# Kernel tuning notes

Measured on AMD Instinct MI355X. Metric: run time of the kernel, lower is better.

Reference implementation:

```python
import jax, jax.numpy as jnp
import numpy as np

B, T, D = 4, 2048, 768
H, HD = 8, 96          # n_heads, head_dim
NB = HD // 24          # number of 24-dim Leech blocks per head
NEG_INF = -1e30


def _leech_kernel_24():
    # QR of the bidiagonal/circulant base matrix, as in generate_leech_kernel
    base = np.zeros((24, 24), dtype=np.float32)
    for i in range(23):
        base[i, i] = 2.0
        base[i, i + 1] = 2.0
    base[23, 23] = 2.0
    base[23, 0] = -2.0
    q, _ = np.linalg.qr(base)
    return jnp.asarray(q, dtype=jnp.float32)


def setup_inputs() -> dict:
    key = jax.random.key(0)
    k1, k2, k3 = jax.random.split(key, 3)
    x = jax.random.normal(k1, (B, T, D), dtype=jnp.float32)
    w_qkv = jax.random.normal(k2, (3 * D, D), dtype=jnp.float32) * (D ** -0.5)
    w_out = jax.random.normal(k3, (D, D), dtype=jnp.float32) * (D ** -0.5)
    kernel = _leech_kernel_24()
    return {"x": x, "w_qkv": w_qkv, "w_out": w_out, "kernel": kernel}


def reference(x, w_qkv, w_out, kernel):
    Bx, Tx, Dx = x.shape
    scale = HD ** -0.5
    # qkv projection (bias=False)
    qkv = jnp.einsum('btd,ed->bte', x, w_qkv)            # [B,T,3D]
    qkv = qkv.reshape(Bx, Tx, 3, H, HD).transpose(2, 0, 3, 1, 4)  # [3,B,H,T,HD]
    q, k, v = qkv[0], qkv[1], qkv[2]
    # per-24-block orthogonal Leech rotation on q and k
    q = jnp.einsum('bhtni,ij->bhtnj', q.reshape(Bx, H, Tx, NB, 24), kernel)
    k = jnp.einsum('bhtni,ij->bhtnj', k.reshape(Bx, H, Tx, NB, 24), kernel)
    q = q.reshape(Bx, H, Tx, HD)
    k = k.reshape(Bx, H, Tx, HD)
    # causal attention (manual softmax; dropout inactive in eval)
    scores = jnp.einsum('bhqd,bhkd->bhqk', q, k) * scale
    causal = jnp.tril(jnp.ones((Tx, Tx), dtype=bool))
    scores = jnp.where(causal[None, None], scores, NEG_INF)
    attn = jax.nn.softmax(scores, axis=-1)
    out = jnp.einsum('bhqk,bhkd->bhqd', attn, v)          # [B,H,T,HD]
    out = out.transpose(0, 2, 1, 3).reshape(Bx, Tx, Dx)
    return jnp.einsum('btd,ed->bte', out, w_out)
```

## Files before the change

### kernel.cpp

```cpp
#include <hip/hip_runtime.h>
#include <cstdint>
#include <cstddef>

#define Bq 4
#define T 2048
#define Dm 768
#define H 8
#define HD 96
#define BH 32
#define QEL ((size_t)BH*T*HD)
#define KEL ((size_t)BH*T*128)
#define PSTRIDE 98304
#define QS 0.14724703336f
#define KVB 64
#define M0 12.0f

typedef unsigned int u32;
typedef unsigned long long u64;
typedef _Float16 f16x8 __attribute__((ext_vector_type(8)));
typedef _Float16 f16x4 __attribute__((ext_vector_type(4)));
typedef float f32x4 __attribute__((ext_vector_type(4)));

__global__ __launch_bounds__(256)
void cvt_tile(const float* __restrict__ in, _Float16* __restrict__ out)
{
    const int tid  = threadIdx.x;
    const int lane = tid & 63;
    const int gw   = (blockIdx.x * 256 + tid) >> 6;
    const int kc   = gw % 96;
    const int row  = (gw / 96) * 64 + lane;
    const float4 a = *reinterpret_cast<const float4*>(in + (size_t)row * 768 + kc * 8);
    const float4 b = *reinterpret_cast<const float4*>(in + (size_t)row * 768 + kc * 8 + 4);
    f16x8 h;
    h[0] = (_Float16)a.x; h[1] = (_Float16)a.y; h[2] = (_Float16)a.z; h[3] = (_Float16)a.w;
    h[4] = (_Float16)b.x; h[5] = (_Float16)b.y; h[6] = (_Float16)b.z; h[7] = (_Float16)b.w;
    *reinterpret_cast<f16x8*>(
        out + (size_t)(row >> 7) * PSTRIDE + (size_t)kc * 1024 + (row & 127) * 8) = h;
}

template <bool SCATTER>
__global__ __launch_bounds__(256)
void gemm_mfma(const _Float16* __restrict__ At, const _Float16* __restrict__ Bt,
               _Float16* __restrict__ qb, _Float16* __restrict__ kpd,
               _Float16* __restrict__ vtb, float* __restrict__ C,
               int N, int nx)
{
    constexpr int NSTEP = Dm / 64;
    __shared__ _Float16 As[2][8 * 128 * 8];
    __shared__ _Float16 Bs[2][8 * 128 * 8];

    const int tid  = threadIdx.x;
    const int lane = tid & 63;
    const int wid  = tid >> 6;
    const int li   = lane & 15;
    const int lg   = lane >> 4;
    const int wr   = wid >> 1;
    const int wc   = wid & 1;

    const int qch = gridDim.x >> 3;
    const int id  = (blockIdx.x & 7) * qch + (blockIdx.x >> 3);
    const int m0  = (id / nx) * 128;
    const int n0  = (id % nx) * 128;

    const _Float16* baseA = At + (size_t)(m0 >> 7) * PSTRIDE;
    const _Float16* baseB = Bt + (size_t)(n0 >> 7) * PSTRIDE;

    f32x4 acc[4][4];
#pragma unroll
    for (int i = 0; i < 4; ++i)
#pragma unroll
        for (int j = 0; j < 4; ++j) acc[i][j] = (f32x4)0.f;

    auto STAGE = [&](int t, int b) {
        const _Float16* pa = baseA + (t << 13);
        const _Float16* pb = baseB + (t << 13);
#pragma unroll
        for (int i = 0; i < 4; ++i) {
            const int s = wid * 64 + i * 256;
            __builtin_amdgcn_global_load_lds(
                (const __attribute__((address_space(1))) void*)(pa + (size_t)(s + lane) * 8),
                (__attribute__((address_space(3))) void*)&As[b][s * 8], 16, 0, 0);
            __builtin_amdgcn_global_load_lds(
                (const __attribute__((address_space(1))) void*)(pb + (size_t)(s + lane) * 8),
                (__attribute__((address_space(3))) void*)&Bs[b][s * 8], 16, 0, 0);
        }
    };

    STAGE(0, 0);
    for (int t = 0; t < NSTEP; ++t) {
        const int p = t & 1;
        if (t + 1 < NSTEP) {
            STAGE(t + 1, p ^ 1);
            asm volatile("s_waitcnt vmcnt(8)" ::: "memory");
        } else {
            asm volatile("s_waitcnt vmcnt(0)" ::: "memory");
        }
        __builtin_amdgcn_s_barrier();

#pragma unroll
        for (int c = 0; c < 2; ++c) {
            f16x8 af[4], bf[4];
#pragma unroll
            for (int i = 0; i < 4; ++i)
                af[i] = *reinterpret_cast<const f16x8*>(
                    &As[p][((c * 4 + lg) * 128 + wr * 64 + i * 16 + li) * 8]);
#pragma unroll
            for (int j = 0; j < 4; ++j)
                bf[j] = *reinterpret_cast<const f16x8*>(
                    &Bs[p][((c * 4 + lg) * 128 + wc * 64 + j * 16 + li) * 8]);
            __builtin_amdgcn_s_setprio(1);
#pragma unroll
            for (int i = 0; i < 4; ++i)
#pragma unroll
                for (int j = 0; j < 4; ++j)
                    acc[i][j] = __builtin_amdgcn_mfma_f32_16x16x32_f16(
                        af[i], bf[j], acc[i][j], 0, 0, 0);
            __builtin_amdgcn_s_setprio(0);
        }

        asm volatile("s_waitcnt lgkmcnt(0)" ::: "memory");
        __builtin_amdgcn_s_barrier();
    }

#pragma unroll
    for (int i = 0; i < 4; ++i) {
#pragma unroll
        for (int r = 0; r < 4; ++r) {
            const int m = m0 + wr * 64 + i * 16 + lg * 4 + r;
            if (SCATTER) {
                const int b_ = m >> 11, t_ = m & 2047;
#pragma unroll
                for (int j = 0; j < 4; ++j) {
                    const int e = n0 + wc * 64 + j * 16 + li;
                    const int c = e / Dm;
                    const int rem = e - c * Dm;
                    const int h = rem / HD;
                    const int d = rem - h * HD;
                    const size_t bhx = (size_t)(b_ * H + h);
                    const float v = acc[i][j][r];
                    if (c == 0)
                        qb[(bhx * T + t_) * HD + d] = (_Float16)(v * QS);
                    else if (c == 1)
                        kpd[(bhx * T + t_) * 128 + d] = (_Float16)v;
                    else
                        vtb[(bhx * 96 + d) * T + t_] = (_Float16)v;
                }
            } else {
#pragma unroll
                for (int j = 0; j < 4; ++j) {
                    const int n = n0 + wc * 64 + j * 16 + li;
                    C[(size_t)m * N + n] = acc[i][j][r];
                }
            }
        }
    }
}

__global__ __launch_bounds__(256)
void attn_mfma(const _Float16* __restrict__ QG, const _Float16* __restrict__ KG,
               const _Float16* __restrict__ VtG, _Float16* __restrict__ aoh)
{
    __shared__ __align__(16) _Float16 Klds[2][64 * 128];
    __shared__ __align__(16) _Float16 Vlds[2][112 * 64];
    __shared__ __align__(16) _Float16 Pl[4][16][72];

    const int tid  = threadIdx.x;
    const int lane = tid & 63;
    const int wid  = tid >> 6;
    const int lg   = lane >> 4;
    const int li   = lane & 15;

    const int bh = blockIdx.x & 31;
    const int i  = blockIdx.x >> 5;
    const int qt0 = i, qt1 = 31 - i;

    {
        const u32 one2 = 0x3C003C00u;
        u32* vp0 = reinterpret_cast<u32*>(&Vlds[0][96 * 64]);
        u32* vp1 = reinterpret_cast<u32*>(&Vlds[1][96 * 64]);
#pragma unroll
        for (int k = tid; k < 512; k += 256) {
            const u32 v = (k < 32) ? one2 : 0u;
            vp0[k] = v; vp1[k] = v;
        }
    }
    __syncthreads();

    f16x8 qf0[3], qf1[3];
    {
        const _Float16* qr0 = QG + ((size_t)bh * T + qt0 * 64 + wid * 16 + li) * HD;
        const _Float16* qr1 = QG + ((size_t)bh * T + qt1 * 64 + wid * 16 + li) * HD;
#pragma unroll
        for (int ch = 0; ch < 3; ++ch) {
            qf0[ch] = *reinterpret_cast<const f16x8*>(qr0 + ch * 32 + lg * 8);
            qf1[ch] = *reinterpret_cast<const f16x8*>(qr1 + ch * 32 + lg * 8);
        }
    }

    const int swz = (li & 7) << 3;
    int kofs[4][3], vofs[7][2];
#pragma unroll
    for (int kt = 0; kt < 4; ++kt)
#pragma unroll
        for (int ch = 0; ch < 3; ++ch)
            kofs[kt][ch] = (kt * 16 + li) * 128 + ((ch * 32 + lg * 8) ^ swz);
#pragma unroll
    for (int dt = 0; dt < 7; ++dt)
#pragma unroll
        for (int pc = 0; pc < 2; ++pc)
            vofs[dt][pc] = (dt * 16 + li) * 64 + ((pc * 32 + lg * 8) ^ swz);

    const int rK = lane >> 4;
    const int cK = (lane & 15) * 8;
    const int rV = lane >> 3;
    const int cV = (lane & 7) * 8;
    auto STAGE = [&](int kb, int b) {
#pragma unroll
        for (int ii = 0; ii < 4; ++ii) {
            const int r  = wid * 16 + ii * 4 + rK;
            const int c0 = cK ^ (((ii * 4 + rK) & 7) << 3);
            const _Float16* src = KG + ((size_t)(bh * T + kb + r)) * 128 + c0;
            __builtin_amdgcn_global_load_lds(
                (const __attribute__((address_space(1))) void*)src,
                (__attribute__((address_space(3))) void*)&Klds[b][(wid * 16 + ii * 4) * 128],
                16, 0, 0);
        }
#pragma unroll
        for (int jj = 0; jj < 3; ++jj) {
            const int r  = wid * 24 + jj * 8 + rV;
            const int c0 = cV ^ (rV << 3);
            const _Float16* src = VtG + ((size_t)(bh * 96 + r)) * T + kb + c0;
            __builtin_amdgcn_global_load_lds(
                (const __attribute__((address_space(1))) void*)src,
                (__attribute__((address_space(3))) void*)&Vlds[b][(wid * 24 + jj * 8) * 64],
                16, 0, 0);
        }
    };

    f32x4 acc0[7], acc1[7];
#pragma unroll
    for (int dt = 0; dt < 7; ++dt) { acc0[dt] = (f32x4)0.f; acc1[dt] = (f32x4)0.f; }

    auto ROUND_FULL = [&](const f16x8 (&qf)[3], f32x4 (&acc)[7],
                          int p, int nextkb) {
        STAGE(nextkb, p ^ 1);
        asm volatile("s_waitcnt vmcnt(7)" ::: "memory");
        __builtin_amdgcn_s_barrier();

        const _Float16* Kb = &Klds[p][0];
        const _Float16* Vb = &Vlds[p][0];

        f16x8 kf[4][3];
#pragma unroll
        for (int kt = 0; kt < 4; ++kt)
#pragma unroll
            for (int ch = 0; ch < 3; ++ch)
                kf[kt][ch] = *reinterpret_cast<const f16x8*>(Kb + kofs[kt][ch]);

        f32x4 st[4];
        __builtin_amdgcn_s_setprio(1);
#pragma unroll
        for (int kt = 0; kt < 4; ++kt) {
            st[kt] = (f32x4)(-M0);
#pragma unroll
            for (int ch = 0; ch < 3; ++ch)
                st[kt] = __builtin_amdgcn_mfma_f32_16x16x32_f16(
                    kf[kt][ch], qf[ch], st[kt], 0, 0, 0);
        }
        __builtin_amdgcn_s_setprio(0);

#pragma unroll
        for (int kt = 0; kt < 4; ++kt) {
            const auto a = __builtin_amdgcn_cvt_pkrtz(
                __builtin_amdgcn_exp2f(st[kt][0]),
                __builtin_amdgcn_exp2f(st[kt][1]));
            const auto b = __builtin_amdgcn_cvt_pkrtz(
                __builtin_amdgcn_exp2f(st[kt][2]),
                __builtin_amdgcn_exp2f(st[kt][3]));
            const u64 w = (u64)__builtin_bit_cast(u32, a) |
                          ((u64)__builtin_bit_cast(u32, b) << 32);
            *reinterpret_cast<u64*>(&Pl[wid][li][kt * 16 + lg * 4]) = w;
        }

#pragma unroll
        for (int pc = 0; pc < 2; ++pc) {
            const f16x8 pf = *reinterpret_cast<const f16x8*>(
                &Pl[wid][li][pc * 32 + lg * 8]);
            __builtin_amdgcn_s_setprio(1);
#pragma unroll
            for (int dt = 0; dt < 7; ++dt) {
                const f16x8 vf = *reinterpret_cast<const f16x8*>(Vb + vofs[dt][pc]);
                acc[dt] = __builtin_amdgcn_mfma_f32_16x16x32_f16(
                    pf, vf, acc[dt], 0, 0, 0);
            }
            __builtin_amdgcn_s_setprio(0);
        }

        asm volatile("s_waitcnt lgkmcnt(0)" ::: "memory");
        __builtin_amdgcn_s_barrier();
    };

    auto ROUND_DIAG = [&](int kb, int q0w, const f16x8 (&qf)[3], f32x4 (&acc)[7],
                          int p, int nextkb, bool has_next) {
        if (has_next) {
            STAGE(nextkb, p ^ 1);
            asm volatile("s_waitcnt vmcnt(7)" ::: "memory");
        } else {
            asm volatile("s_waitcnt vmcnt(0)" ::: "memory");
        }
        __builtin_amdgcn_s_barrier();

        const _Float16* Kb = &Klds[p][0];
        const _Float16* Vb = &Vlds[p][0];
        const int nkt = min(4, ((q0w + 15 - kb) >> 4) + 1);

        f16x8 kf[4][3];
#pragma unroll
        for (int kt = 0; kt < 4; ++kt)
            if (kt < nkt) {
#pragma unroll
                for (int ch = 0; ch < 3; ++ch)
                    kf[kt][ch] = *reinterpret_cast<const f16x8*>(Kb + kofs[kt][ch]);
            }

        f32x4 st[4];
        __builtin_amdgcn_s_setprio(1);
#pragma unroll
        for (int kt = 0; kt < 4; ++kt) {
            st[kt] = (f32x4)(-M0);
            if (kt < nkt) {
#pragma unroll
                for (int ch = 0; ch < 3; ++ch)
                    st[kt] = __builtin_amdgcn_mfma_f32_16x16x32_f16(
                        kf[kt][ch], qf[ch], st[kt], 0, 0, 0);
            }
        }
        __builtin_amdgcn_s_setprio(0);

        const int qg = q0w + li;
#pragma unroll
        for (int kt = 0; kt < 4; ++kt)
            if (kt < nkt && kb + kt * 16 + 15 > q0w) {
#pragma unroll
                for (int rr = 0; rr < 4; ++rr) {
                    const int kg = kb + kt * 16 + lg * 4 + rr;
                    if (kg > qg) st[kt][rr] = -1e30f;
                }
            }

#pragma unroll
        for (int kt = 0; kt < 4; ++kt)
            if (kt < nkt) {
                const auto a = __builtin_amdgcn_cvt_pkrtz(
                    __builtin_amdgcn_exp2f(st[kt][0]),
                    __builtin_amdgcn_exp2f(st[kt][1]));
                const auto b = __builtin_amdgcn_cvt_pkrtz(
                    __builtin_amdgcn_exp2f(st[kt][2]),
                    __builtin_amdgcn_exp2f(st[kt][3]));
                const u64 w = (u64)__builtin_bit_cast(u32, a) |
                              ((u64)__builtin_bit_cast(u32, b) << 32);
                *reinterpret_cast<u64*>(&Pl[wid][li][kt * 16 + lg * 4]) = w;
            }
        if (nkt & 1)
            *reinterpret_cast<u64*>(&Pl[wid][li][nkt * 16 + lg * 4]) = 0ull;

        const int npc = (nkt + 1) >> 1;
#pragma unroll
        for (int pc = 0; pc < 2; ++pc)
            if (pc < npc) {
                const f16x8 pf = *reinterpret_cast<const f16x8*>(
                    &Pl[wid][li][pc * 32 + lg * 8]);
                __builtin_amdgcn_s_setprio(1);
#pragma unroll
                for (int dt = 0; dt < 7; ++dt) {
                    const f16x8 vf = *reinterpret_cast<const f16x8*>(Vb + vofs[dt][pc]);
                    acc[dt] = __builtin_amdgcn_mfma_f32_16x16x32_f16(
                        pf, vf, acc[dt], 0, 0, 0);
                }
                __builtin_amdgcn_s_setprio(0);
            }

        asm volatile("s_waitcnt lgkmcnt(0)" ::: "memory");
        __builtin_amdgcn_s_barrier();
    };

    STAGE(0, 0);
    const int q0w0 = qt0 * 64 + wid * 16;
    const int q0w1 = qt1 * 64 + wid * 16;
    int r = 0;
    for (int t = 0; t < i; ++t, ++r)
        ROUND_FULL(qf0, acc0, r & 1, (t + 1) * KVB);
    ROUND_DIAG(i * KVB, q0w0, qf0, acc0, r & 1, 0, true); ++r;
    for (int t = 0; t < 31 - i; ++t, ++r)
        ROUND_FULL(qf1, acc1, r & 1, (t + 1) * KVB);
    ROUND_DIAG((31 - i) * KVB, q0w1, qf1, acc1, r & 1, 0, false);

    const int ob = bh >> 3, oh = bh & 7;
#pragma unroll
    for (int rr = 0; rr < 4; ++rr) {
        {
            const float l    = __shfl(acc0[6][rr], lg << 4);
            const float linv = 1.0f / l;
            const int m = ob * T + qt0 * 64 + wid * 16 + lg * 4 + rr;
            _Float16* op = aoh + (size_t)(m >> 7) * PSTRIDE + (size_t)(m & 127) * 8
                         + (size_t)(oh * 12 + (li >> 3)) * 1024 + (li & 7);
#pragma unroll
            for (int dt = 0; dt < 6; ++dt)
                op[dt * 2048] = (_Float16)(acc0[dt][rr] * linv);
        }
        {
            const float l    = __shfl(acc1[6][rr], lg << 4);
            const float linv = 1.0f / l;
            const int m = ob * T + qt1 * 64 + wid * 16 + lg * 4 + rr;
            _Float16* op = aoh + (size_t)(m >> 7) * PSTRIDE + (size_t)(m & 127) * 8
                         + (size_t)(oh * 12 + (li >> 3)) * 1024 + (li & 7);
#pragma unroll
            for (int dt = 0; dt < 6; ++dt)
                op[dt * 2048] = (_Float16)(acc1[dt][rr] * linv);
        }
    }
}

extern "C" void kernel_launch(void* const* d_in, const int* in_sizes, int n_in,
                              void* d_out, int out_size, void* d_ws, size_t ws_size,
                              hipStream_t stream)
{
    const float* x     = (const float*)d_in[0];
    const float* w_qkv = (const float*)d_in[1];
    const float* w_out = (const float*)d_in[2];

    _Float16* qb  = (_Float16*)d_ws;
    _Float16* kpd = qb + QEL;
    _Float16* vtb = kpd + KEL;
    _Float16* aoh = vtb + QEL;
    _Float16* xh  = aoh + (size_t)Bq * T * Dm;
    _Float16* wqh = xh + (size_t)Bq * T * Dm;
    _Float16* woh = wqh + (size_t)3 * Dm * Dm;
    float* out = (float*)d_out;

    const int M = Bq * T;

    cvt_tile<<<dim3(M * 96 / 256), dim3(256), 0, stream>>>(x, xh);
    cvt_tile<<<dim3(3 * Dm * 96 / 256), dim3(256), 0, stream>>>(w_qkv, wqh);
    cvt_tile<<<dim3(Dm * 96 / 256), dim3(256), 0, stream>>>(w_out, woh);

    gemm_mfma<true><<<dim3((3 * Dm / 128) * (M / 128)), dim3(256), 0, stream>>>(
        xh, wqh, qb, kpd, vtb, nullptr, 3 * Dm, 3 * Dm / 128);

    attn_mfma<<<dim3(BH * (T / 128)), dim3(256), 0, stream>>>(qb, kpd, vtb, aoh);

    gemm_mfma<false><<<dim3((Dm / 128) * (M / 128)), dim3(256), 0, stream>>>(
        aoh, woh, nullptr, nullptr, nullptr, out, Dm, Dm / 128);
}
```

Baseline: 148.0 us.

## Process 128-row query tiles per block so each K/V tile feeds two query sub-tiles

Each wave now handles 32 query rows (two 16-row sub-tiles) instead of 16, so every K and V fragment read from LDS drives two MFMAs. The grid shrinks from 512 to 256 blocks, and causal pairing uses 128-row tiles (i and 15-i). This halves LDS K/V traffic and global staging per unit of work. In exchange it raises register pressure from doubled accumulators and query fragments, and halves the number of blocks, which may reduce occupancy and load balance on the GPU.

Result: slower. 154.0 us (+4.0%).

```diff
diff --git a/kernel.cpp b/kernel.cpp
--- a/kernel.cpp
+++ b/kernel.cpp
@@ -162,7 +162,7 @@
 {
     __shared__ __align__(16) _Float16 Klds[2][64 * 128];
     __shared__ __align__(16) _Float16 Vlds[2][112 * 64];
-    __shared__ __align__(16) _Float16 Pl[4][16][72];
+    __shared__ __align__(16) _Float16 Pl[4][32][72];
 
     const int tid  = threadIdx.x;
     const int lane = tid & 63;
@@ -172,7 +172,7 @@
 
     const int bh = blockIdx.x & 31;
     const int i  = blockIdx.x >> 5;
-    const int qt0 = i, qt1 = 31 - i;
+    const int qt0 = i, qt1 = 15 - i;
 
     {
         const u32 one2 = 0x3C003C00u;
@@ -185,17 +185,6 @@
         }
     }
     __syncthreads();
-
-    f16x8 qf0[3], qf1[3];
-    {
-        const _Float16* qr0 = QG + ((size_t)bh * T + qt0 * 64 + wid * 16 + li) * HD;
-        const _Float16* qr1 = QG + ((size_t)bh * T + qt1 * 64 + wid * 16 + li) * HD;
-#pragma unroll
-        for (int ch = 0; ch < 3; ++ch) {
-            qf0[ch] = *reinterpret_cast<const f16x8*>(qr0 + ch * 32 + lg * 8);
-            qf1[ch] = *reinterpret_cast<const f16x8*>(qr1 + ch * 32 + lg * 8);
-        }
-    }
 
     const int swz = (li & 7) << 3;
     int kofs[4][3], vofs[7][2];
@@ -237,12 +226,27 @@
         }
     };
 
-    f32x4 acc0[7], acc1[7];
-#pragma unroll
-    for (int dt = 0; dt < 7; ++dt) { acc0[dt] = (f32x4)0.f; acc1[dt] = (f32x4)0.f; }
-
-    auto ROUND_FULL = [&](const f16x8 (&qf)[3], f32x4 (&acc)[7],
-                          int p, int nextkb) {
+    f16x8 qf[2][3];
+    auto LOADQ = [&](int qtile) {
+#pragma unroll
+        for (int qt = 0; qt < 2; ++qt) {
+            const _Float16* qrow =
+                QG + ((size_t)bh * T + qtile * 128 + wid * 32 + qt * 16 + li) * HD;
+#pragma unroll
+            for (int ch = 0; ch < 3; ++ch)
+                qf[qt][ch] = *reinterpret_cast<const f16x8*>(qrow + ch * 32 + lg * 8);
+        }
+    };
+
+    f32x4 acc[2][7];
+    auto ZACC = [&]() {
+#pragma unroll
+        for (int qt = 0; qt < 2; ++qt)
+#pragma unroll
+            for (int dt = 0; dt < 7; ++dt) acc[qt][dt] = (f32x4)0.f;
+    };
+
+    auto ROUND_FULL = [&](int p, int nextkb) {
         STAGE(nextkb, p ^ 1);
         asm volatile("s_waitcnt vmcnt(7)" ::: "memory");
         __builtin_amdgcn_s_barrier();
@@ -250,48 +254,49 @@
         const _Float16* Kb = &Klds[p][0];
         const _Float16* Vb = &Vlds[p][0];
 
-        f16x8 kf[4][3];
-#pragma unroll
-        for (int kt = 0; kt < 4; ++kt)
-#pragma unroll
-            for (int ch = 0; ch < 3; ++ch)
-                kf[kt][ch] = *reinterpret_cast<const f16x8*>(Kb + kofs[kt][ch]);
-
-        f32x4 st[4];
+        f32x4 st[2][4];
         __builtin_amdgcn_s_setprio(1);
 #pragma unroll
         for (int kt = 0; kt < 4; ++kt) {
-            st[kt] = (f32x4)(-M0);
-#pragma unroll
-            for (int ch = 0; ch < 3; ++ch)
-                st[kt] = __builtin_amdgcn_mfma_f32_16x16x32_f16(
-                    kf[kt][ch], qf[ch], st[kt], 0, 0, 0);
+            const f16x8 k0 = *reinterpret_cast<const f16x8*>(Kb + kofs[kt][0]);
+            const f16x8 k1 = *reinterpret_cast<const f16x8*>(Kb + kofs[kt][1]);
+            const f16x8 k2 = *reinterpret_cast<const f16x8*>(Kb + kofs[kt][2]);
+            st[0][kt] = __builtin_amdgcn_mfma_f32_16x16x32_f16(k0, qf[0][0], (f32x4)(-M0), 0, 0, 0);
+            st[1][kt] = __builtin_amdgcn_mfma_f32_16x16x32_f16(k0, qf[1][0], (f32x4)(-M0), 0, 0, 0);
+            st[0][kt] = __builtin_amdgcn_mfma_f32_16x16x32_f16(k1, qf[0][1], st[0][kt], 0, 0, 0);
+            st[1][kt] = __builtin_amdgcn_mfma_f32_16x16x32_f16(k1, qf[1][1], st[1][kt], 0, 0, 0);
+            st[0][kt] = __builtin_amdgcn_mfma_f32_16x16x32_f16(k2, qf[0][2], st[0][kt], 0, 0, 0);
+            st[1][kt] = __builtin_amdgcn_mfma_f32_16x16x32_f16(k2, qf[1][2], st[1][kt], 0, 0, 0);
         }
         __builtin_amdgcn_s_setprio(0);
 
 #pragma unroll
-        for (int kt = 0; kt < 4; ++kt) {
-            const auto a = __builtin_amdgcn_cvt_pkrtz(
-                __builtin_amdgcn_exp2f(st[kt][0]),
-                __builtin_amdgcn_exp2f(st[kt][1]));
-            const auto b = __builtin_amdgcn_cvt_pkrtz(
-                __builtin_amdgcn_exp2f(st[kt][2]),
-                __builtin_amdgcn_exp2f(st[kt][3]));
-            const u64 w = (u64)__builtin_bit_cast(u32, a) |
-                          ((u64)__builtin_bit_cast(u32, b) << 32);
-            *reinterpret_cast<u64*>(&Pl[wid][li][kt * 16 + lg * 4]) = w;
-        }
+        for (int qt = 0; qt < 2; ++qt)
+#pragma unroll
+            for (int kt = 0; kt < 4; ++kt) {
+                const auto a = __builtin_amdgcn_cvt_pkrtz(
+                    __builtin_amdgcn_exp2f(st[qt][kt][0]),
+                    __builtin_amdgcn_exp2f(st[qt][kt][1]));
+                const auto b = __builtin_amdgcn_cvt_pkrtz(
+                    __builtin_amdgcn_exp2f(st[qt][kt][2]),
+                    __builtin_amdgcn_exp2f(st[qt][kt][3]));
+                const u64 w = (u64)__builtin_bit_cast(u32, a) |
+                              ((u64)__builtin_bit_cast(u32, b) << 32);
+                *reinterpret_cast<u64*>(&Pl[wid][qt * 16 + li][kt * 16 + lg * 4]) = w;
+            }
 
 #pragma unroll
         for (int pc = 0; pc < 2; ++pc) {
-            const f16x8 pf = *reinterpret_cast<const f16x8*>(
+            const f16x8 pf0 = *reinterpret_cast<const f16x8*>(
                 &Pl[wid][li][pc * 32 + lg * 8]);
+            const f16x8 pf1 = *reinterpret_cast<const f16x8*>(
+                &Pl[wid][16 + li][pc * 32 + lg * 8]);
             __builtin_amdgcn_s_setprio(1);
 #pragma unroll
             for (int dt = 0; dt < 7; ++dt) {
                 const f16x8 vf = *reinterpret_cast<const f16x8*>(Vb + vofs[dt][pc]);
-                acc[dt] = __builtin_amdgcn_mfma_f32_16x16x32_f16(
-                    pf, vf, acc[dt], 0, 0, 0);
+                acc[0][dt] = __builtin_amdgcn_mfma_f32_16x16x32_f16(pf0, vf, acc[0][dt], 0, 0, 0);
+                acc[1][dt] = __builtin_amdgcn_mfma_f32_16x16x32_f16(pf1, vf, acc[1][dt], 0, 0, 0);
             }
             __builtin_amdgcn_s_setprio(0);
         }
@@ -300,8 +305,7 @@
         __builtin_amdgcn_s_barrier();
     };
 
-    auto ROUND_DIAG = [&](int kb, int q0w, const f16x8 (&qf)[3], f32x4 (&acc)[7],
-                          int p, int nextkb, bool has_next) {
+    auto ROUND_DIAG = [&](int kb, int q0base, int p, int nextkb, bool has_next) {
         if (has_next) {
             STAGE(nextkb, p ^ 1);
             asm volatile("s_waitcnt vmcnt(7)" ::: "memory");
@@ -312,70 +316,83 @@
 
         const _Float16* Kb = &Klds[p][0];
         const _Float16* Vb = &Vlds[p][0];
-        const int nkt = min(4, ((q0w + 15 - kb) >> 4) + 1);
-
-        f16x8 kf[4][3];
-#pragma unroll
-        for (int kt = 0; kt < 4; ++kt)
-            if (kt < nkt) {
-#pragma unroll
-                for (int ch = 0; ch < 3; ++ch)
-                    kf[kt][ch] = *reinterpret_cast<const f16x8*>(Kb + kofs[kt][ch]);
-            }
-
-        f32x4 st[4];
+        const int q0w0 = q0base + wid * 32;
+        int nkt[2];
+        nkt[0] = min(4, ((q0w0 + 15 - kb) >> 4) + 1);
+        nkt[1] = min(4, ((q0w0 + 31 - kb) >> 4) + 1);
+        const int nktmax = nkt[1];
+
+        f32x4 st[2][4];
         __builtin_amdgcn_s_setprio(1);
 #pragma unroll
         for (int kt = 0; kt < 4; ++kt) {
-            st[kt] = (f32x4)(-M0);
-            if (kt < nkt) {
-#pragma unroll
-                for (int ch = 0; ch < 3; ++ch)
-                    st[kt] = __builtin_amdgcn_mfma_f32_16x16x32_f16(
-                        kf[kt][ch], qf[ch], st[kt], 0, 0, 0);
+            st[0][kt] = (f32x4)(-M0);
+            st[1][kt] = (f32x4)(-M0);
+            if (kt < nktmax) {
+                const f16x8 k0 = *reinterpret_cast<const f16x8*>(Kb + kofs[kt][0]);
+                const f16x8 k1 = *reinterpret_cast<const f16x8*>(Kb + kofs[kt][1]);
+                const f16x8 k2 = *reinterpret_cast<const f16x8*>(Kb + kofs[kt][2]);
+                st[1][kt] = __builtin_amdgcn_mfma_f32_16x16x32_f16(k0, qf[1][0], st[1][kt], 0, 0, 0);
+                st[1][kt] = __builtin_amdgcn_mfma_f32_16x16x32_f16(k1, qf[1][1], st[1][kt], 0, 0, 0);
+                st[1][kt] = __builtin_amdgcn_mfma_f32_16x16x32_f16(k2, qf[1][2], st[1][kt], 0, 0, 0);
+                if (kt < nkt[0]) {
+                    st[0][kt] = __builtin_amdgcn_mfma_f32_16x16x32_f16(k0, qf[0][0], st[0][kt], 0, 0, 0);
+                    st[0][kt] = __builtin_amdgcn_mfma_f32_16x16x32_f16(k1, qf[0][1], st[0][kt], 0, 0, 0);
+                    st[0][kt] = __builtin_amdgcn_mfma_f32_16x16x32_f16(k2, qf[0][2], st[0][kt], 0, 0, 0);
+                }
             }
         }
         __builtin_amdgcn_s_setprio(0);
 
-        const int qg = q0w + li;
-#pragma unroll
-        for (int kt = 0; kt < 4; ++kt)
-            if (kt < nkt && kb + kt * 16 + 15 > q0w) {
-#pragma unroll
-                for (int rr = 0; rr < 4; ++rr) {
-                    const int kg = kb + kt * 16 + lg * 4 + rr;
-                    if (kg > qg) st[kt][rr] = -1e30f;
-                }
-            }
-
-#pragma unroll
-        for (int kt = 0; kt < 4; ++kt)
-            if (kt < nkt) {
-                const auto a = __builtin_amdgcn_cvt_pkrtz(
-                    __builtin_amdgcn_exp2f(st[kt][0]),
-                    __builtin_amdgcn_exp2f(st[kt][1]));
-                const auto b = __builtin_amdgcn_cvt_pkrtz(
-                    __builtin_amdgcn_exp2f(st[kt][2]),
-                    __builtin_amdgcn_exp2f(st[kt][3]));
-                const u64 w = (u64)__builtin_bit_cast(u32, a) |
-                              ((u64)__builtin_bit_cast(u32, b) << 32);
-                *reinterpret_cast<u64*>(&Pl[wid][li][kt * 16 + lg * 4]) = w;
-            }
-        if (nkt & 1)
-            *reinterpret_cast<u64*>(&Pl[wid][li][nkt * 16 + lg * 4]) = 0ull;
-
-        const int npc = (nkt + 1) >> 1;
+#pragma unroll
+        for (int qt = 0; qt < 2; ++qt) {
+            const int q0w = q0w0 + qt * 16;
+            const int qg  = q0w + li;
+#pragma unroll
+            for (int kt = 0; kt < 4; ++kt)
+                if (kt < nkt[qt] && kb + kt * 16 + 15 > q0w) {
+#pragma unroll
+                    for (int rr = 0; rr < 4; ++rr) {
+                        const int kg = kb + kt * 16 + lg * 4 + rr;
+                        if (kg > qg) st[qt][kt][rr] = -1e30f;
+                    }
+                }
+#pragma unroll
+            for (int kt = 0; kt < 4; ++kt)
+                if (kt < nkt[qt]) {
+                    const auto a = __builtin_amdgcn_cvt_pkrtz(
+                        __builtin_amdgcn_exp2f(st[qt][kt][0]),
+                        __builtin_amdgcn_exp2f(st[qt][kt][1]));
+                    const auto b = __builtin_amdgcn_cvt_pkrtz(
+                        __builtin_amdgcn_exp2f(st[qt][kt][2]),
+                        __builtin_amdgcn_exp2f(st[qt][kt][3]));
+                    const u64 w = (u64)__builtin_bit_cast(u32, a) |
+                                  ((u64)__builtin_bit_cast(u32, b) << 32);
+                    *reinterpret_cast<u64*>(&Pl[wid][qt * 16 + li][kt * 16 + lg * 4]) = w;
+                }
+            if (nkt[qt] > 0 && (nkt[qt] & 1))
+                *reinterpret_cast<u64*>(&Pl[wid][qt * 16 + li][nkt[qt] * 16 + lg * 4]) = 0ull;
+        }
+
+        const int npc0 = (nkt[0] + 1) >> 1;
+        const int npc1 = (nkt[1] + 1) >> 1;
 #pragma unroll
         for (int pc = 0; pc < 2; ++pc)
-            if (pc < npc) {
-                const f16x8 pf = *reinterpret_cast<const f16x8*>(
-                    &Pl[wid][li][pc * 32 + lg * 8]);
+            if (pc < npc1) {
+                const f16x8 pf1 = *reinterpret_cast<const f16x8*>(
+                    &Pl[wid][16 + li][pc * 32 + lg * 8]);
+                f16x8 pf0;
+                const bool do0 = (pc < npc0);
+                if (do0)
+                    pf0 = *reinterpret_cast<const f16x8*>(
+                        &Pl[wid][li][pc * 32 + lg * 8]);
                 __builtin_amdgcn_s_setprio(1);
 #pragma unroll
                 for (int dt = 0; dt < 7; ++dt) {
                     const f16x8 vf = *reinterpret_cast<const f16x8*>(Vb + vofs[dt][pc]);
-                    acc[dt] = __builtin_amdgcn_mfma_f32_16x16x32_f16(
-                        pf, vf, acc[dt], 0, 0, 0);
+                    acc[1][dt] = __builtin_amdgcn_mfma_f32_16x16x32_f16(pf1, vf, acc[1][dt], 0, 0, 0);
+                    if (do0)
+                        acc[0][dt] = __builtin_amdgcn_mfma_f32_16x16x32_f16(pf0, vf, acc[0][dt], 0, 0, 0);
                 }
                 __builtin_amdgcn_s_setprio(0);
             }
@@ -384,41 +401,42 @@
         __builtin_amdgcn_s_barrier();
     };
 
+    const int ob = bh >> 3, oh = bh & 7;
+    auto EPI = [&](int qtile) {
+#pragma unroll
+        for (int qt = 0; qt < 2; ++qt)
+#pragma unroll
+            for (int rr = 0; rr < 4; ++rr) {
+                const float l    = __shfl(acc[qt][6][rr], lg << 4);
+                const float linv = 1.0f / l;
+                const int m = ob * T + qtile * 128 + wid * 32 + qt * 16 + lg * 4 + rr;
+                _Float16* op = aoh + (size_t)(m >> 7) * PSTRIDE + (size_t)(m & 127) * 8
+                             + (size_t)(oh * 12 + (li >> 3)) * 1024 + (li & 7);
+#pragma unroll
+                for (int dt = 0; dt < 6; ++dt)
+                    op[dt * 2048] = (_Float16)(acc[qt][dt][rr] * linv);
+            }
+    };
+
     STAGE(0, 0);
-    const int q0w0 = qt0 * 64 + wid * 16;
-    const int q0w1 = qt1 * 64 + wid * 16;
+    LOADQ(qt0);
+    ZACC();
     int r = 0;
-    for (int t = 0; t < i; ++t, ++r)
-        ROUND_FULL(qf0, acc0, r & 1, (t + 1) * KVB);
-    ROUND_DIAG(i * KVB, q0w0, qf0, acc0, r & 1, 0, true); ++r;
-    for (int t = 0; t < 31 - i; ++t, ++r)
-        ROUND_FULL(qf1, acc1, r & 1, (t + 1) * KVB);
-    ROUND_DIAG((31 - i) * KVB, q0w1, qf1, acc1, r & 1, 0, false);
-
-    const int ob = bh >> 3, oh = bh & 7;
-#pragma unroll
-    for (int rr = 0; rr < 4; ++rr) {
-        {
-            const float l    = __shfl(acc0[6][rr], lg << 4);
-            const float linv = 1.0f / l;
-            const int m = ob * T + qt0 * 64 + wid * 16 + lg * 4 + rr;
-            _Float16* op = aoh + (size_t)(m >> 7) * PSTRIDE + (size_t)(m & 127) * 8
-                         + (size_t)(oh * 12 + (li >> 3)) * 1024 + (li & 7);
-#pragma unroll
-            for (int dt = 0; dt < 6; ++dt)
-                op[dt * 2048] = (_Float16)(acc0[dt][rr] * linv);
-        }
-        {
-            const float l    = __shfl(acc1[6][rr], lg << 4);
-            const float linv = 1.0f / l;
-            const int m = ob * T + qt1 * 64 + wid * 16 + lg * 4 + rr;
-            _Float16* op = aoh + (size_t)(m >> 7) * PSTRIDE + (size_t)(m & 127) * 8
-                         + (size_t)(oh * 12 + (li >> 3)) * 1024 + (li & 7);
-#pragma unroll
-            for (int dt = 0; dt < 6; ++dt)
-                op[dt * 2048] = (_Float16)(acc1[dt][rr] * linv);
-        }
-    }
+    const int nf0 = 2 * i;
+    for (int t = 0; t < nf0; ++t, ++r)
+        ROUND_FULL(r & 1, (t + 1) * KVB);
+    ROUND_DIAG(nf0 * KVB, qt0 * 128, r & 1, (nf0 + 1) * KVB, true); ++r;
+    ROUND_DIAG((nf0 + 1) * KVB, qt0 * 128, r & 1, 0, true); ++r;
+    EPI(qt0);
+
+    LOADQ(qt1);
+    ZACC();
+    const int nf1 = 30 - 2 * i;
+    for (int t = 0; t < nf1; ++t, ++r)
+        ROUND_FULL(r & 1, (t + 1) * KVB);
+    ROUND_DIAG(nf1 * KVB, qt1 * 128, r & 1, (nf1 + 1) * KVB, true); ++r;
+    ROUND_DIAG((nf1 + 1) * KVB, qt1 * 128, r & 1, 0, false); ++r;
+    EPI(qt1);
 }
 
 extern "C" void kernel_launch(void* const* d_in, const int* in_sizes, int n_in,
@@ -447,7 +465,7 @@
     gemm_mfma<true><<<dim3((3 * Dm / 128) * (M / 128)), dim3(256), 0, stream>>>(
         xh, wqh, qb, kpd, vtb, nullptr, 3 * Dm, 3 * Dm / 128);
 
-    attn_mfma<<<dim3(BH * (T / 128)), dim3(256), 0, stream>>>(qb, kpd, vtb, aoh);
+    attn_mfma<<<dim3(BH * 8), dim3(256), 0, stream>>>(qb, kpd, vtb, aoh);
 
     gemm_mfma<false><<<dim3((Dm / 128) * (M / 128)), dim3(256), 0, stream>>>(
         aoh, woh, nullptr, nullptr, nullptr, out, Dm, Dm / 128);
```
